# Kernel optimization log

Measured on AMD Instinct MI355X. Metric: run time of the kernel, lower is better.

Reference implementation:

```python
import jax, jax.numpy as jnp
import numpy as np

B, S, D = 4, 2048, 1024
H, DK = 16, 64

def setup_inputs() -> dict:
    key = jax.random.key(0)
    ks = jax.random.split(key, 11)
    s_in = 1.0 / np.sqrt(D)      # torch Linear default init scale ~ U(-1/sqrt(fan_in),..)
    s_out = 1.0 / np.sqrt(H * DK)
    return {
        "q_in": jax.random.normal(ks[0], (B, S, D), jnp.float32),
        "k_in": jax.random.normal(ks[1], (B, S, D), jnp.float32),
        "v_in": jax.random.normal(ks[2], (B, S, D), jnp.float32),
        # per-head projection weights, stacked over heads: [H, D, DK]
        "wq": jax.random.uniform(ks[3], (H, D, DK), jnp.float32, -s_in, s_in),
        "bq": jax.random.uniform(ks[4], (H, DK), jnp.float32, -s_in, s_in),
        "wk": jax.random.uniform(ks[5], (H, D, DK), jnp.float32, -s_in, s_in),
        "bk": jax.random.uniform(ks[6], (H, DK), jnp.float32, -s_in, s_in),
        "wv": jax.random.uniform(ks[7], (H, D, DK), jnp.float32, -s_in, s_in),
        "bv": jax.random.uniform(ks[8], (H, DK), jnp.float32, -s_in, s_in),
        # output linear: [H*DK, D]
        "wo": jax.random.uniform(ks[9], (H * DK, D), jnp.float32, -s_out, s_out),
        "bo": jax.random.uniform(ks[10], (D,), jnp.float32, -s_out, s_out),
    }

def reference(q_in, k_in, v_in, wq, bq, wk, bk, wv, bv, wo, bo):
    # per-head projections, batched over heads: [B,H,S,DK]
    q = jnp.einsum("bsd,hdk->bhsk", q_in, wq) + bq[None, :, None, :]
    k = jnp.einsum("bsd,hdk->bhsk", k_in, wk) + bk[None, :, None, :]
    v = jnp.einsum("bsd,hdk->bhsk", v_in, wv) + bv[None, :, None, :]
    scale = q.shape[-1] ** 0.5
    scores = jnp.einsum("bhsk,bhtk->bhst", q, k) / scale  # [B,H,S,S]
    attn = jax.nn.softmax(scores, axis=-1)
    out = jnp.einsum("bhst,bhtk->bhsk", attn, v)           # [B,H,S,DK]
    # concat heads along last dim (head-major order matches torch.cat over heads)
    cat = jnp.transpose(out, (0, 2, 1, 3)).reshape(B, S, H * DK)
    return cat @ wo + bo
```

## Files before the change

### kernel.cpp

```cpp
#include <hip/hip_runtime.h>
#include <hip/hip_bf16.h>
#include <math.h>

typedef short bf16x8 __attribute__((ext_vector_type(8)));
typedef unsigned short us8 __attribute__((ext_vector_type(8)));
typedef unsigned short us4 __attribute__((ext_vector_type(4)));
typedef float f32x4 __attribute__((ext_vector_type(4)));
typedef float f32x16 __attribute__((ext_vector_type(16)));
typedef unsigned int u32;
typedef unsigned int u32x4 __attribute__((ext_vector_type(4)));

__device__ __forceinline__ unsigned short f2bf(float f) {
  unsigned int u = __builtin_bit_cast(unsigned int, f);
  u += 0x7fffu + ((u >> 16) & 1u);
  return (unsigned short)(u >> 16);
}

__device__ __forceinline__ void gload16(const void* g, void* l) {
  __builtin_amdgcn_global_load_lds(
      (const __attribute__((address_space(1))) unsigned int*)g,
      (__attribute__((address_space(3))) unsigned int*)l, 16, 0, 0);
}

__global__ __launch_bounds__(256) void k_conv3(const float* __restrict__ i0,
                                               const float* __restrict__ i1,
                                               const float* __restrict__ i2,
                                               unsigned short* __restrict__ o0,
                                               unsigned short* __restrict__ o1,
                                               unsigned short* __restrict__ o2) {
  int bid = blockIdx.x;
  int g = bid >> 13;
  const float* in = g == 0 ? i0 : g == 1 ? i1 : i2;
  unsigned short* out = g == 0 ? o0 : g == 1 ? o1 : o2;
  int i = (bid & 8191) * 256 + threadIdx.x;
  float4 v = ((const float4*)in)[i];
  us4 o;
  o[0] = f2bf(v.x); o[1] = f2bf(v.y); o[2] = f2bf(v.z); o[3] = f2bf(v.w);
  ((us4*)out)[i] = o;
}

__global__ __launch_bounds__(256) void k_pack4(const float* __restrict__ wq,
                                               const float* __restrict__ wk,
                                               const float* __restrict__ wv,
                                               const float* __restrict__ wo,
                                               unsigned short* __restrict__ Wqt,
                                               unsigned short* __restrict__ Wkt,
                                               unsigned short* __restrict__ Wvt,
                                               unsigned short* __restrict__ Wot) {
  __shared__ float tl[64][65];
  int bid = blockIdx.x;
  int g = bid >> 8;
  int bl = bid & 255;
  int tid = threadIdx.x;
  if (g < 3) {
    const float* w = g == 0 ? wq : g == 1 ? wk : wv;
    unsigned short* wt = g == 0 ? Wqt : g == 1 ? Wkt : Wvt;
    int h = bl >> 4, dt = bl & 15;
#pragma unroll
    for (int i = 0; i < 16; ++i) {
      int idx = i * 256 + tid;
      int d = idx >> 6, c = idx & 63;
      tl[c][d] = w[h * 65536 + (dt * 64 + d) * 64 + c];
    }
    __syncthreads();
#pragma unroll
    for (int i = 0; i < 16; ++i) {
      int idx = i * 256 + tid;
      int c = idx >> 6, d = idx & 63;
      wt[(h * 64 + c) * 1024 + dt * 64 + d] = f2bf(tl[c][d]);
    }
  } else {
    int kt = bl >> 4, nt = bl & 15;
#pragma unroll
    for (int i = 0; i < 16; ++i) {
      int idx = i * 256 + tid;
      int k = idx >> 6, n = idx & 63;
      tl[n][k] = wo[(kt * 64 + k) * 1024 + nt * 64 + n];
    }
    __syncthreads();
#pragma unroll
    for (int i = 0; i < 16; ++i) {
      int idx = i * 256 + tid;
      int n = idx >> 6, k = idx & 63;
      Wot[(nt * 64 + n) * 1024 + kt * 64 + k] = f2bf(tl[n][k]);
    }
  }
}

template<int OUT_BF16>
__device__ __forceinline__ void gemm_body(const unsigned short* __restrict__ A,
                                          const unsigned short* __restrict__ Bt,
                                          const float* __restrict__ bias,
                                          void* __restrict__ Cout, float scale,
                                          int bid) {
  __shared__ unsigned short As[128 * 32];
  __shared__ unsigned short Bs[128 * 32];
  const int tid = threadIdx.x;
  const int l = tid & 63, w = tid >> 6;
  const int wr = w >> 1, wc = w & 1;
  bid = (bid & 7) * 64 + (bid >> 3);
  const int bx = bid & 7;
  const int by = bid >> 3;
  const long brow = (long)by * 128;
  const int bcol = bx * 128;
  const int lr = l & 15, lg = l >> 4;
  f32x4 acc[4][4] = {};

  for (int k0 = 0; k0 < 1024; k0 += 32) {
    __syncthreads();
#pragma unroll
    for (int i = 0; i < 2; ++i) {
      int idx = i * 256 + tid;
      int r = idx >> 2, ch = idx & 3;
      gload16(A + (brow + r) * 1024 + k0 + ch * 8, &As[(i * 256 + w * 64) * 8]);
      gload16(Bt + (long)(bcol + r) * 1024 + k0 + ch * 8, &Bs[(i * 256 + w * 64) * 8]);
    }
    __syncthreads();
    bf16x8 af[4], bfr[4];
#pragma unroll
    for (int m = 0; m < 4; ++m)
      af[m] = *(const bf16x8*)&As[(wr * 64 + m * 16 + lr) * 32 + lg * 8];
#pragma unroll
    for (int n = 0; n < 4; ++n)
      bfr[n] = *(const bf16x8*)&Bs[(wc * 64 + n * 16 + lr) * 32 + lg * 8];
#pragma unroll
    for (int m = 0; m < 4; ++m)
#pragma unroll
      for (int n = 0; n < 4; ++n)
        acc[m][n] = __builtin_amdgcn_mfma_f32_16x16x32_bf16(af[m], bfr[n], acc[m][n], 0, 0, 0);
  }

#pragma unroll
  for (int m = 0; m < 4; ++m) {
#pragma unroll
    for (int n = 0; n < 4; ++n) {
      int col = bcol + wc * 64 + n * 16 + lr;
      float bia = bias[col];
#pragma unroll
      for (int i = 0; i < 4; ++i) {
        long row = brow + wr * 64 + m * 16 + lg * 4 + i;
        float v = (acc[m][n][i] + bia) * scale;
        if (OUT_BF16) ((unsigned short*)Cout)[row * 1024 + col] = f2bf(v);
        else          ((float*)Cout)[row * 1024 + col] = v;
      }
    }
  }
}

__global__ __launch_bounds__(256) void k_gemm_qkv(const unsigned short* __restrict__ Aq,
                                                  const unsigned short* __restrict__ Ak,
                                                  const unsigned short* __restrict__ Av,
                                                  const unsigned short* __restrict__ Wqt,
                                                  const unsigned short* __restrict__ Wkt,
                                                  const unsigned short* __restrict__ Wvt,
                                                  const float* __restrict__ bq,
                                                  const float* __restrict__ bk,
                                                  const float* __restrict__ bv,
                                                  unsigned short* __restrict__ Qa,
                                                  unsigned short* __restrict__ Ka,
                                                  unsigned short* __restrict__ Va,
                                                  float qscale) {
  int g = blockIdx.x >> 9;
  int bl = blockIdx.x & 511;
  const unsigned short* A  = g == 0 ? Aq  : g == 1 ? Ak  : Av;
  const unsigned short* Bt = g == 0 ? Wqt : g == 1 ? Wkt : Wvt;
  const float* bia         = g == 0 ? bq  : g == 1 ? bk  : bv;
  unsigned short* C        = g == 0 ? Qa  : g == 1 ? Ka  : Va;
  gemm_body<1>(A, Bt, bia, C, g == 0 ? qscale : 1.0f, bl);
}

__global__ __launch_bounds__(256) void k_gemm_wo(const unsigned short* __restrict__ A,
                                                 const unsigned short* __restrict__ Bt,
                                                 const float* __restrict__ bias,
                                                 float* __restrict__ Cout) {
  gemm_body<0>(A, Bt, bias, Cout, 1.0f, blockIdx.x);
}

__global__ __launch_bounds__(256) void k_transpose_v(const unsigned short* __restrict__ V,
                                                     unsigned short* __restrict__ Vt) {
  __shared__ unsigned short tile[64][72];
  int bid = blockIdx.x;
  int bh = bid >> 5, st = bid & 31;
  int b = bh >> 4, h = bh & 15;
  int tid = threadIdx.x;
#pragma unroll
  for (int i = 0; i < 2; ++i) {
    int idx = i * 256 + tid;
    int r = idx >> 3, ch = idx & 7;
    us8 v = *(const us8*)&V[((long)(b * 2048 + st * 64 + r)) * 1024 + h * 64 + ch * 8];
#pragma unroll
    for (int j = 0; j < 8; ++j) tile[ch * 8 + j][r] = v[j];
  }
  __syncthreads();
#pragma unroll
  for (int i = 0; i < 2; ++i) {
    int idx = i * 256 + tid;
    int c = idx >> 3, ch = idx & 7;
    us8 v;
#pragma unroll
    for (int j = 0; j < 8; ++j) v[j] = tile[c][ch * 8 + j];
    *(us8*)&Vt[(long)bh * 131072 + (long)c * 2048 + st * 64 + ch * 8] = v;
  }
}

__global__ __launch_bounds__(256) void k_attn3(const unsigned short* __restrict__ Q,
                                               const unsigned short* __restrict__ K,
                                               const unsigned short* __restrict__ Vt,
                                               unsigned short* __restrict__ AO) {
  __shared__ unsigned short Ks[2][64 * 64];
  __shared__ unsigned short Vs[2][64 * 64];
  __shared__ float Li[4][32];
  const int tid = threadIdx.x;
  const int l = tid & 63, w = tid >> 6;
  const int l31 = l & 31, hi = l >> 5;
  int bid0 = blockIdx.x;
  int bid = (bid0 & 7) * 128 + (bid0 >> 3);
  const int bh = bid >> 4, qt0 = bid & 15;
  const int b = bh >> 4, h = bh & 15;
  const unsigned short* Qb = Q + (long)b * 2048 * 1024 + h * 64;
  const unsigned short* Kb = K + (long)b * 2048 * 1024 + h * 64;
  const unsigned short* Vb = Vt + (long)bh * 131072;
  const int qbase = qt0 * 128 + w * 32;

  bf16x8 qf[4];
#pragma unroll
  for (int c = 0; c < 4; ++c)
    qf[c] = *(const bf16x8*)&Qb[(long)(qbase + l31) * 1024 + c * 16 + hi * 8];

  f32x16 acc[2] = {};
  f32x4 li4 = {0.f, 0.f, 0.f, 0.f};
  const int rsw = (l31 & 7) << 4;

  auto stage = [&](int buf, int t0) {
#pragma unroll
    for (int i = 0; i < 2; ++i) {
      int idx = i * 256 + tid;
      int r = idx >> 3, ch = idx & 7;
      int sw = (ch * 16) ^ ((r & 7) << 4);
      gload16((const char*)(Kb + (long)(t0 + r) * 1024) + sw, (char*)&Ks[buf][0] + idx * 16);
      gload16((const char*)(Vb + (long)r * 2048 + t0) + sw, (char*)&Vs[buf][0] + idx * 16);
    }
  };

  stage(0, 0);
  int cur = 0;
  for (int t0 = 0; t0 < 2048; t0 += 64) {
    __syncthreads();
    if (t0 + 64 < 2048) stage(cur ^ 1, t0 + 64);

    const char* Kc = (const char*)&Ks[cur][0];
    const char* Vc = (const char*)&Vs[cur][0];

    bf16x8 paf[4];
#pragma unroll
    for (int h2 = 0; h2 < 2; ++h2) {
      bf16x8 kf[4];
#pragma unroll
      for (int c = 0; c < 4; ++c)
        kf[c] = *(const bf16x8*)(Kc + (h2 * 32 + l31) * 128 + ((c * 32 + hi * 16) ^ rsw));
      f32x16 s = {};
#pragma unroll
      for (int c = 0; c < 4; ++c)
        s = __builtin_amdgcn_mfma_f32_32x32x16_bf16(kf[c], qf[c], s, 0, 0, 0);
      float p[16];
#pragma unroll
      for (int r = 0; r < 16; ++r) p[r] = __builtin_amdgcn_exp2f(s[r]);
#pragma unroll
      for (int r = 0; r < 16; ++r) li4[r & 3] += p[r];
      u32 wg[4][2];
#pragma unroll
      for (int g = 0; g < 4; ++g) {
        asm("v_cvt_pk_bf16_f32 %0, %1, %2" : "=v"(wg[g][0]) : "v"(p[4 * g]), "v"(p[4 * g + 1]));
        asm("v_cvt_pk_bf16_f32 %0, %1, %2" : "=v"(wg[g][1]) : "v"(p[4 * g + 2]), "v"(p[4 * g + 3]));
      }
#pragma unroll
      for (int sub = 0; sub < 2; ++sub) {
        u32 x0 = wg[2 * sub][0], y0 = wg[2 * sub + 1][0];
        u32 x1 = wg[2 * sub][1], y1 = wg[2 * sub + 1][1];
        asm("v_permlane32_swap_b32 %0, %1" : "+v"(x0), "+v"(y0));
        asm("v_permlane32_swap_b32 %0, %1" : "+v"(x1), "+v"(y1));
        u32x4 fw; fw[0] = x0; fw[1] = x1; fw[2] = y0; fw[3] = y1;
        paf[h2 * 2 + sub] = __builtin_bit_cast(bf16x8, fw);
      }
    }
#pragma unroll
    for (int ck = 0; ck < 4; ++ck)
#pragma unroll
      for (int ct = 0; ct < 2; ++ct) {
        bf16x8 vf = *(const bf16x8*)(Vc + (ct * 32 + l31) * 128 + ((ck * 32 + hi * 16) ^ rsw));
        acc[ct] = __builtin_amdgcn_mfma_f32_32x32x16_bf16(paf[ck], vf, acc[ct], 0, 0, 0);
      }
    cur ^= 1;
  }

  float li = li4[0] + li4[1] + li4[2] + li4[3];
  li += __shfl_xor(li, 32);
  if (hi == 0) Li[w][l31] = 1.f / li;
#pragma unroll
  for (int ct = 0; ct < 2; ++ct)
#pragma unroll
    for (int r = 0; r < 16; ++r) {
      int qrow = (r & 3) + 8 * (r >> 2) + 4 * hi;
      float inv = Li[w][qrow];
      long row = (long)b * 2048 + qbase + qrow;
      int col = h * 64 + ct * 32 + l31;
      AO[row * 1024 + col] = f2bf(acc[ct][r] * inv);
    }
}

extern "C" void kernel_launch(void* const* d_in, const int* in_sizes, int n_in,
                              void* d_out, int out_size, void* d_ws, size_t ws_size,
                              hipStream_t stream) {
  (void)in_sizes; (void)n_in; (void)out_size; (void)ws_size;
  const float* q_in = (const float*)d_in[0];
  const float* k_in = (const float*)d_in[1];
  const float* v_in = (const float*)d_in[2];
  const float* wq   = (const float*)d_in[3];
  const float* bq   = (const float*)d_in[4];
  const float* wk   = (const float*)d_in[5];
  const float* bk   = (const float*)d_in[6];
  const float* wv   = (const float*)d_in[7];
  const float* bv   = (const float*)d_in[8];
  const float* wo   = (const float*)d_in[9];
  const float* bo   = (const float*)d_in[10];

  char* ws = (char*)d_ws;
  const size_t SZA = (size_t)8192 * 1024 * 2;
  unsigned short* Aq  = (unsigned short*)(ws);
  unsigned short* Ak  = (unsigned short*)(ws + SZA);
  unsigned short* Av  = (unsigned short*)(ws + 2 * SZA);
  unsigned short* Qa  = (unsigned short*)(ws + 3 * SZA);
  unsigned short* Ka  = (unsigned short*)(ws + 4 * SZA);
  unsigned short* Va  = (unsigned short*)(ws + 5 * SZA);
  unsigned short* Wqt = (unsigned short*)(ws + 6 * SZA);
  unsigned short* Wkt = Wqt + 1048576;
  unsigned short* Wvt = Wkt + 1048576;
  unsigned short* Wot = Wvt + 1048576;
  unsigned short* Vtr = Ak;
  unsigned short* AO  = Aq;

  const float QSCALE = 0.1803368801111204f;

  k_conv3<<<24576, 256, 0, stream>>>(q_in, k_in, v_in, Aq, Ak, Av);
  k_pack4<<<1024, 256, 0, stream>>>(wq, wk, wv, wo, Wqt, Wkt, Wvt, Wot);
  k_gemm_qkv<<<1536, 256, 0, stream>>>(Aq, Ak, Av, Wqt, Wkt, Wvt, bq, bk, bv,
                                       Qa, Ka, Va, QSCALE);
  k_transpose_v<<<2048, 256, 0, stream>>>(Va, Vtr);
  k_attn3<<<1024, 256, 0, stream>>>(Qa, Ka, Vtr, AO);
  k_gemm_wo<<<512, 256, 0, stream>>>(AO, Wot, bo, (float*)d_out);
}
```

Baseline: 357.8 us.

## Double-buffer GEMM LDS tiles and hoist address math in attention loop

The GEMM body moves from a single LDS buffer with two barriers per k-step to a double-buffered tile, so the next tile's global-to-LDS load is issued before computing on the current one. Addresses are precomputed as pointers that advance each step. The attention kernel keeps its K/V double buffering but switches to precomputed incrementing pointers, an unrolled two-phase loop and a zero-init first MFMA. Row sums are accumulated in packed float2 vectors. This doubles GEMM LDS use, which may reduce occupancy.

Measured after the change: 357.6 us. About the same (-0.1%).

```diff
diff --git a/kernel.cpp b/kernel.cpp
--- a/kernel.cpp
+++ b/kernel.cpp
@@ -5,6 +5,7 @@
 typedef short bf16x8 __attribute__((ext_vector_type(8)));
 typedef unsigned short us8 __attribute__((ext_vector_type(8)));
 typedef unsigned short us4 __attribute__((ext_vector_type(4)));
+typedef float f32x2 __attribute__((ext_vector_type(2)));
 typedef float f32x4 __attribute__((ext_vector_type(4)));
 typedef float f32x16 __attribute__((ext_vector_type(16)));
 typedef unsigned int u32;
@@ -93,8 +94,8 @@
                                           const float* __restrict__ bias,
                                           void* __restrict__ Cout, float scale,
                                           int bid) {
-  __shared__ unsigned short As[128 * 32];
-  __shared__ unsigned short Bs[128 * 32];
+  __shared__ unsigned short As[2][128 * 32];
+  __shared__ unsigned short Bs[2][128 * 32];
   const int tid = threadIdx.x;
   const int l = tid & 63, w = tid >> 6;
   const int wr = w >> 1, wc = w & 1;
@@ -106,28 +107,43 @@
   const int lr = l & 15, lg = l >> 4;
   f32x4 acc[4][4] = {};
 
-  for (int k0 = 0; k0 < 1024; k0 += 32) {
-    __syncthreads();
-#pragma unroll
-    for (int i = 0; i < 2; ++i) {
-      int idx = i * 256 + tid;
-      int r = idx >> 2, ch = idx & 3;
-      gload16(A + (brow + r) * 1024 + k0 + ch * 8, &As[(i * 256 + w * 64) * 8]);
-      gload16(Bt + (long)(bcol + r) * 1024 + k0 + ch * 8, &Bs[(i * 256 + w * 64) * 8]);
-    }
-    __syncthreads();
-    bf16x8 af[4], bfr[4];
-#pragma unroll
-    for (int m = 0; m < 4; ++m)
-      af[m] = *(const bf16x8*)&As[(wr * 64 + m * 16 + lr) * 32 + lg * 8];
-#pragma unroll
-    for (int n = 0; n < 4; ++n)
-      bfr[n] = *(const bf16x8*)&Bs[(wc * 64 + n * 16 + lr) * 32 + lg * 8];
-#pragma unroll
-    for (int m = 0; m < 4; ++m)
+  const char* aS0 = (const char*)(A + (brow + (tid >> 2)) * 1024 + (tid & 3) * 8);
+  const char* aS1 = aS0 + 131072;
+  const char* bS0 = (const char*)(Bt + (long)(bcol + (tid >> 2)) * 1024 + (tid & 3) * 8);
+  const char* bS1 = bS0 + 131072;
+  char* aD = (char*)&As[0][0] + w * 1024;
+  char* bD = (char*)&Bs[0][0] + w * 1024;
+  const char* aP = (const char*)&As[0][0] + ((wr * 64 + lr) * 32 + lg * 8) * 2;
+  const char* bP = (const char*)&Bs[0][0] + ((wc * 64 + lr) * 32 + lg * 8) * 2;
+
+  auto stage = [&](int curbuf) {
+    gload16(aS0, aD + curbuf * 8192);
+    gload16(aS1, aD + curbuf * 8192 + 4096);
+    gload16(bS0, bD + curbuf * 8192);
+    gload16(bS1, bD + curbuf * 8192 + 4096);
+    aS0 += 64; aS1 += 64; bS0 += 64; bS1 += 64;
+  };
+
+  stage(0);
+  for (int kk = 0; kk < 16; ++kk) {
+#pragma unroll
+    for (int cur = 0; cur < 2; ++cur) {
+      int k0 = kk * 64 + cur * 32;
+      __syncthreads();
+      if (k0 + 32 < 1024) stage(cur ^ 1);
+      bf16x8 af[4], bfr[4];
+#pragma unroll
+      for (int m = 0; m < 4; ++m)
+        af[m] = *(const bf16x8*)(aP + cur * 8192 + m * 1024);
 #pragma unroll
       for (int n = 0; n < 4; ++n)
-        acc[m][n] = __builtin_amdgcn_mfma_f32_16x16x32_bf16(af[m], bfr[n], acc[m][n], 0, 0, 0);
+        bfr[n] = *(const bf16x8*)(bP + cur * 8192 + n * 1024);
+#pragma unroll
+      for (int m = 0; m < 4; ++m)
+#pragma unroll
+        for (int n = 0; n < 4; ++n)
+          acc[m][n] = __builtin_amdgcn_mfma_f32_16x16x32_bf16(af[m], bfr[n], acc[m][n], 0, 0, 0);
+    }
   }
 
 #pragma unroll
@@ -203,12 +219,11 @@
   }
 }
 
-__global__ __launch_bounds__(256) void k_attn3(const unsigned short* __restrict__ Q,
+__global__ __launch_bounds__(256) void k_attn4(const unsigned short* __restrict__ Q,
                                                const unsigned short* __restrict__ K,
                                                const unsigned short* __restrict__ Vt,
                                                unsigned short* __restrict__ AO) {
-  __shared__ unsigned short Ks[2][64 * 64];
-  __shared__ unsigned short Vs[2][64 * 64];
+  __shared__ unsigned short KV[4][4096];
   __shared__ float Li[4][32];
   const int tid = threadIdx.x;
   const int l = tid & 63, w = tid >> 6;
@@ -228,72 +243,87 @@
     qf[c] = *(const bf16x8*)&Qb[(long)(qbase + l31) * 1024 + c * 16 + hi * 8];
 
   f32x16 acc[2] = {};
-  f32x4 li4 = {0.f, 0.f, 0.f, 0.f};
+  f32x16 z16 = {};
+  f32x2 li2a = {0.f, 0.f}, li2b = {0.f, 0.f};
   const int rsw = (l31 & 7) << 4;
 
-  auto stage = [&](int buf, int t0) {
-#pragma unroll
-    for (int i = 0; i < 2; ++i) {
-      int idx = i * 256 + tid;
-      int r = idx >> 3, ch = idx & 7;
-      int sw = (ch * 16) ^ ((r & 7) << 4);
-      gload16((const char*)(Kb + (long)(t0 + r) * 1024) + sw, (char*)&Ks[buf][0] + idx * 16);
-      gload16((const char*)(Vb + (long)r * 2048 + t0) + sw, (char*)&Vs[buf][0] + idx * 16);
-    }
+  const char* pb[4];
+#pragma unroll
+  for (int c = 0; c < 4; ++c)
+    pb[c] = (const char*)&KV[0][0] + l31 * 128 + ((c * 32 + hi * 16) ^ rsw);
+
+  const int sch = tid & 7, srw = tid >> 3;
+  const int ssw = (sch * 16) ^ ((srw & 7) << 4);
+  const char* ks0 = (const char*)Kb + (long)srw * 2048 + ssw;
+  const char* ks1 = ks0 + 65536;
+  const char* vs0 = (const char*)Vb + (long)srw * 4096 + ssw;
+  const char* vs1 = vs0 + 131072;
+  char* dK = (char*)&KV[0][0] + w * 1024;
+  char* dV = dK + 8192;
+
+  auto stage = [&](int buf) {
+    gload16(ks0, dK + buf * 16384);
+    gload16(ks1, dK + buf * 16384 + 4096);
+    gload16(vs0, dV + buf * 16384);
+    gload16(vs1, dV + buf * 16384 + 4096);
+    ks0 += 131072; ks1 += 131072;
+    vs0 += 128;    vs1 += 128;
   };
 
-  stage(0, 0);
-  int cur = 0;
-  for (int t0 = 0; t0 < 2048; t0 += 64) {
-    __syncthreads();
-    if (t0 + 64 < 2048) stage(cur ^ 1, t0 + 64);
-
-    const char* Kc = (const char*)&Ks[cur][0];
-    const char* Vc = (const char*)&Vs[cur][0];
-
-    bf16x8 paf[4];
-#pragma unroll
-    for (int h2 = 0; h2 < 2; ++h2) {
-      bf16x8 kf[4];
-#pragma unroll
-      for (int c = 0; c < 4; ++c)
-        kf[c] = *(const bf16x8*)(Kc + (h2 * 32 + l31) * 128 + ((c * 32 + hi * 16) ^ rsw));
-      f32x16 s = {};
-#pragma unroll
-      for (int c = 0; c < 4; ++c)
-        s = __builtin_amdgcn_mfma_f32_32x32x16_bf16(kf[c], qf[c], s, 0, 0, 0);
-      float p[16];
-#pragma unroll
-      for (int r = 0; r < 16; ++r) p[r] = __builtin_amdgcn_exp2f(s[r]);
-#pragma unroll
-      for (int r = 0; r < 16; ++r) li4[r & 3] += p[r];
-      u32 wg[4][2];
-#pragma unroll
-      for (int g = 0; g < 4; ++g) {
-        asm("v_cvt_pk_bf16_f32 %0, %1, %2" : "=v"(wg[g][0]) : "v"(p[4 * g]), "v"(p[4 * g + 1]));
-        asm("v_cvt_pk_bf16_f32 %0, %1, %2" : "=v"(wg[g][1]) : "v"(p[4 * g + 2]), "v"(p[4 * g + 3]));
+  stage(0);
+  for (int it = 0; it < 16; ++it) {
+#pragma unroll
+    for (int cur = 0; cur < 2; ++cur) {
+      __syncthreads();
+      if (it < 15 || cur == 0) stage(cur ^ 1);
+
+      bf16x8 paf[4];
+#pragma unroll
+      for (int h2 = 0; h2 < 2; ++h2) {
+        bf16x8 kf[4];
+#pragma unroll
+        for (int c = 0; c < 4; ++c)
+          kf[c] = *(const bf16x8*)(pb[c] + cur * 16384 + h2 * 4096);
+        f32x16 s = __builtin_amdgcn_mfma_f32_32x32x16_bf16(kf[0], qf[0], z16, 0, 0, 0);
+#pragma unroll
+        for (int c = 1; c < 4; ++c)
+          s = __builtin_amdgcn_mfma_f32_32x32x16_bf16(kf[c], qf[c], s, 0, 0, 0);
+        float p[16];
+#pragma unroll
+        for (int r = 0; r < 16; ++r) p[r] = __builtin_amdgcn_exp2f(s[r]);
+#pragma unroll
+        for (int g = 0; g < 4; ++g) {
+          f32x2 pa; pa[0] = p[4 * g]; pa[1] = p[4 * g + 1];
+          f32x2 pc; pc[0] = p[4 * g + 2]; pc[1] = p[4 * g + 3];
+          li2a += pa; li2b += pc;
+        }
+        u32 wg[4][2];
+#pragma unroll
+        for (int g = 0; g < 4; ++g) {
+          asm("v_cvt_pk_bf16_f32 %0, %1, %2" : "=v"(wg[g][0]) : "v"(p[4 * g]), "v"(p[4 * g + 1]));
+          asm("v_cvt_pk_bf16_f32 %0, %1, %2" : "=v"(wg[g][1]) : "v"(p[4 * g + 2]), "v"(p[4 * g + 3]));
+        }
+#pragma unroll
+        for (int sub = 0; sub < 2; ++sub) {
+          u32 x0 = wg[2 * sub][0], y0 = wg[2 * sub + 1][0];
+          u32 x1 = wg[2 * sub][1], y1 = wg[2 * sub + 1][1];
+          asm("v_permlane32_swap_b32 %0, %1" : "+v"(x0), "+v"(y0));
+          asm("v_permlane32_swap_b32 %0, %1" : "+v"(x1), "+v"(y1));
+          u32x4 fw; fw[0] = x0; fw[1] = x1; fw[2] = y0; fw[3] = y1;
+          paf[h2 * 2 + sub] = __builtin_bit_cast(bf16x8, fw);
+        }
       }
 #pragma unroll
-      for (int sub = 0; sub < 2; ++sub) {
-        u32 x0 = wg[2 * sub][0], y0 = wg[2 * sub + 1][0];
-        u32 x1 = wg[2 * sub][1], y1 = wg[2 * sub + 1][1];
-        asm("v_permlane32_swap_b32 %0, %1" : "+v"(x0), "+v"(y0));
-        asm("v_permlane32_swap_b32 %0, %1" : "+v"(x1), "+v"(y1));
-        u32x4 fw; fw[0] = x0; fw[1] = x1; fw[2] = y0; fw[3] = y1;
-        paf[h2 * 2 + sub] = __builtin_bit_cast(bf16x8, fw);
-      }
-    }
-#pragma unroll
-    for (int ck = 0; ck < 4; ++ck)
-#pragma unroll
-      for (int ct = 0; ct < 2; ++ct) {
-        bf16x8 vf = *(const bf16x8*)(Vc + (ct * 32 + l31) * 128 + ((ck * 32 + hi * 16) ^ rsw));
-        acc[ct] = __builtin_amdgcn_mfma_f32_32x32x16_bf16(paf[ck], vf, acc[ct], 0, 0, 0);
-      }
-    cur ^= 1;
-  }
-
-  float li = li4[0] + li4[1] + li4[2] + li4[3];
+      for (int ck = 0; ck < 4; ++ck)
+#pragma unroll
+        for (int ct = 0; ct < 2; ++ct) {
+          bf16x8 vf = *(const bf16x8*)(pb[ck] + cur * 16384 + 8192 + ct * 4096);
+          acc[ct] = __builtin_amdgcn_mfma_f32_32x32x16_bf16(paf[ck], vf, acc[ct], 0, 0, 0);
+        }
+    }
+  }
+
+  float li = li2a[0] + li2a[1] + li2b[0] + li2b[1];
   li += __shfl_xor(li, 32);
   if (hi == 0) Li[w][l31] = 1.f / li;
 #pragma unroll
@@ -346,6 +376,6 @@
   k_gemm_qkv<<<1536, 256, 0, stream>>>(Aq, Ak, Av, Wqt, Wkt, Wvt, bq, bk, bv,
                                        Qa, Ka, Va, QSCALE);
   k_transpose_v<<<2048, 256, 0, stream>>>(Va, Vtr);
-  k_attn3<<<1024, 256, 0, stream>>>(Qa, Ka, Vtr, AO);
+  k_attn4<<<1024, 256, 0, stream>>>(Qa, Ka, Vtr, AO);
   k_gemm_wo<<<512, 256, 0, stream>>>(AO, Wot, bo, (float*)d_out);
 }
```
